# Kernel tuning notes

Hardware: AMD Instinct MI355X
Metric: run time of the kernel (lower is better)

Reference implementation:

```python
import jax, jax.numpy as jnp
import numpy as np

N_NODES = 100000
N_EDGES = 3200000
IN_FEAT = 512
HIDDEN = 16
N_CLASSES = 7


def gcn_conv(x, src, dst, dinv, W, b, n):
    # x: [N, Fin], src/dst: [E+N] (self-loops appended), dinv: [E+N already-indexed? no]
    h = x @ W  # [N, Fout]
    norm = (dinv[src] * dinv[dst])[:, None]  # [E+N, 1]
    msg = h[src] * norm
    out = jax.ops.segment_sum(msg, dst, num_segments=n)
    return out + b


def setup_inputs() -> dict:
    key = jax.random.key(0)
    k1, k2, k3, k4 = jax.random.split(key, 4)
    x = jax.random.normal(k1, (N_NODES, IN_FEAT), dtype=jnp.float32)
    edge_index = jax.random.randint(k2, (2, N_EDGES), 0, N_NODES, dtype=jnp.int64)
    # Glorot-style init for GCNConv linear layers
    W1 = jax.random.normal(k3, (IN_FEAT, HIDDEN), dtype=jnp.float32) / np.sqrt(IN_FEAT)
    b1 = jnp.zeros((HIDDEN,), dtype=jnp.float32)
    W2 = jax.random.normal(k4, (HIDDEN, N_CLASSES), dtype=jnp.float32) / np.sqrt(HIDDEN)
    b2 = jnp.zeros((N_CLASSES,), dtype=jnp.float32)
    return {"x": x, "edge_index": edge_index, "W1": W1, "b1": b1, "W2": W2, "b2": b2}


def reference(x, edge_index, W1, b1, W2, b2):
    n = x.shape[0]
    loop = jnp.arange(n, dtype=edge_index.dtype)
    src = jnp.concatenate([edge_index[0], loop])  # add self-loops (PyG default)
    dst = jnp.concatenate([edge_index[1], loop])
    # symmetric normalization: deg computed on destination with self-loops
    deg = jax.ops.segment_sum(jnp.ones_like(dst, dtype=x.dtype), dst, num_segments=n)
    dinv = jnp.where(deg > 0, jax.lax.rsqrt(deg), 0.0)
    h = gcn_conv(x, src, dst, dinv, W1, b1, n)
    h = jax.nn.relu(h)
    h = gcn_conv(h, src, dst, dinv, W2, b2, n)
    return jax.nn.log_softmax(h, axis=1)
```

## Files before the change

kernel.cpp:

```cpp
#include <hip/hip_runtime.h>

#define IN_FEAT 512
#define HID 16
#define NC 7

#define NPB    128
#define NPB_SH 7
#define NBMAX  1024
#define CAPB   5120
#define CAPS   8192
#define P1_EDGES 8192
#define P1_EPT   32

typedef float fv4 __attribute__((ext_vector_type(4)));

__global__ __launch_bounds__(256) void k_bin2(const int* __restrict__ src,
                                              const int* __restrict__ dst,
                                              int* __restrict__ gcur,
                                              int* __restrict__ binned,
                                              int E, int NB) {
    __shared__ int lcur[NBMAX];
    __shared__ int sbase[NBMAX];
    int tid = threadIdx.x;
    for (int b = tid; b < NB; b += 256) lcur[b] = 0;
    __syncthreads();

    int base = blockIdx.x * P1_EDGES + tid;
    int d[P1_EPT];
    int lp[P1_EPT];
#pragma unroll
    for (int i = 0; i < P1_EPT; ++i) {
        int e = base + i * 256;
        d[i] = (e < E) ? __builtin_nontemporal_load(dst + e) : -1;
    }
#pragma unroll
    for (int i = 0; i < P1_EPT; ++i) {
        if (d[i] >= 0) lp[i] = atomicAdd(&lcur[d[i] >> NPB_SH], 1);
    }
    __syncthreads();
    for (int b = tid; b < NB; b += 256) {
        int c = lcur[b];
        sbase[b] = c ? atomicAdd(&gcur[b], c) : 0;
    }
    __syncthreads();
#pragma unroll
    for (int i = 0; i < P1_EPT; ++i) {
        if (d[i] < 0) continue;
        int e = base + i * 256;
        int s = __builtin_nontemporal_load(src + e);
        int b = d[i] >> NPB_SH;
        int pos = sbase[b] + lp[i];
        if (pos < CAPB)
            binned[(size_t)b * CAPB + pos] = s | ((d[i] & (NPB - 1)) << 20);
    }
}

__global__ __launch_bounds__(1024) void k_bscan(const int* __restrict__ gcur,
                                                int* __restrict__ boff,
                                                int* __restrict__ off,
                                                int NB, int n, int E) {
    __shared__ int wsum[16];
    int tid = threadIdx.x, lane = tid & 63, wid = tid >> 6;
    int v = (tid < NB) ? gcur[tid] : 0;
    int incl = v;
#pragma unroll
    for (int o = 1; o < 64; o <<= 1) {
        int t = __shfl_up(incl, o, 64);
        if (lane >= o) incl += t;
    }
    if (lane == 63) wsum[wid] = incl;
    __syncthreads();
    int wpre = 0;
    for (int k = 0; k < wid; ++k) wpre += wsum[k];
    int ex = wpre + incl - v;
    if (tid < NB) boff[tid] = ex;
    if (tid == 0) off[n] = E;
}

__global__ __launch_bounds__(256) void k_sort2(const int* __restrict__ binned,
                                               const int* __restrict__ gcur,
                                               const int* __restrict__ boff,
                                               int* __restrict__ off,
                                               float* __restrict__ dinv,
                                               int* __restrict__ csr,
                                               const int* __restrict__ src,
                                               const int* __restrict__ dst,
                                               int n, int E) {
    __shared__ int hist[NPB];
    __shared__ int hoff[NPB];
    __shared__ int cur[NPB];
    __shared__ int wtot[2];
    __shared__ int stage[CAPS];
    int b = blockIdx.x;
    int lo = b << NPB_SH;
    int nn = min(NPB, n - lo);
    int tid = threadIdx.x;
    int tot = gcur[b];
    int base = boff[b];
    bool fits = (tot <= CAPB) && (tot <= CAPS);
    if (tid < NPB) { hist[tid] = 0; cur[tid] = 0; }
    __syncthreads();

    const int* bb = binned + (size_t)b * CAPB;
    if (fits) {
        for (int k = tid; k < tot; k += 256)
            atomicAdd(&hist[(bb[k] >> 20) & (NPB - 1)], 1);
    } else {
        for (int e = tid; e < E; e += 256) {
            int dd = dst[e];
            if ((dd >> NPB_SH) == b) atomicAdd(&hist[dd & (NPB - 1)], 1);
        }
    }
    __syncthreads();

    int v = 0, incl = 0;
    if (tid < NPB) {
        v = hist[tid];
        incl = v;
#pragma unroll
        for (int o = 1; o < 64; o <<= 1) {
            int t = __shfl_up(incl, o, 64);
            if ((tid & 63) >= o) incl += t;
        }
        if ((tid & 63) == 63) wtot[tid >> 6] = incl;
    }
    __syncthreads();
    if (tid < NPB) {
        int ex = incl - v + ((tid >= 64) ? wtot[0] : 0);
        hoff[tid] = ex;
        if (tid < nn) {
            off[lo + tid] = base + ex;
            dinv[lo + tid] = rsqrtf((float)v + 1.0f);
        }
    }
    __syncthreads();

    if (fits) {
        for (int k = tid; k < tot; k += 256) {
            int e = bb[k];
            int dl = (e >> 20) & (NPB - 1);
            int p = hoff[dl] + atomicAdd(&cur[dl], 1);
            stage[p] = e & 0xFFFFF;
        }
        __syncthreads();
        for (int k = tid; k < tot; k += 256) csr[base + k] = stage[k];
    } else {
        for (int e = tid; e < E; e += 256) {
            int dd = dst[e];
            if ((dd >> NPB_SH) == b) {
                int dl = dd & (NPB - 1);
                int p = base + hoff[dl] + atomicAdd(&cur[dl], 1);
                csr[p] = src[e];
            }
        }
    }
}

__global__ void k_gemm1(const float* __restrict__ x, const float* __restrict__ W,
                        float* __restrict__ h1, int n) {
    int row = blockIdx.x * blockDim.x + threadIdx.x;
    if (row >= n) return;
    const float4* xr = reinterpret_cast<const float4*>(x + (size_t)row * IN_FEAT);
    float acc[HID];
#pragma unroll
    for (int c = 0; c < HID; ++c) acc[c] = 0.0f;
    for (int kt0 = 0; kt0 < IN_FEAT / 4; kt0 += 8) {
        float4 xv[8];
#pragma unroll
        for (int j = 0; j < 8; ++j) xv[j] = xr[kt0 + j];
#pragma unroll
        for (int j = 0; j < 8; ++j) {
            const float* wk = W + (size_t)(kt0 + j) * 4 * HID;
#pragma unroll
            for (int c = 0; c < HID; ++c) acc[c] = fmaf(xv[j].x, wk[c], acc[c]);
#pragma unroll
            for (int c = 0; c < HID; ++c) acc[c] = fmaf(xv[j].y, wk[HID + c], acc[c]);
#pragma unroll
            for (int c = 0; c < HID; ++c) acc[c] = fmaf(xv[j].z, wk[2 * HID + c], acc[c]);
#pragma unroll
            for (int c = 0; c < HID; ++c) acc[c] = fmaf(xv[j].w, wk[3 * HID + c], acc[c]);
        }
    }
    float4* hp = reinterpret_cast<float4*>(h1 + (size_t)row * HID);
#pragma unroll
    for (int j = 0; j < 4; ++j)
        hp[j] = make_float4(acc[4 * j], acc[4 * j + 1], acc[4 * j + 2], acc[4 * j + 3]);
}

__global__ void k_gather1(const float* __restrict__ h1, const int* __restrict__ csr_src,
                          const int* __restrict__ off, const float* __restrict__ dinv,
                          const float* __restrict__ b1, const float* __restrict__ W2,
                          float* __restrict__ h2, int n) {
    int t = blockIdx.x * blockDim.x + threadIdx.x;
    int v = t >> 2, part = t & 3;
    if (v >= n) return;
    float di = dinv[v];
    float4 hv = reinterpret_cast<const float4*>(h1 + (size_t)v * HID)[part];
    float dw = di * di;
    float4 acc = make_float4(hv.x * dw, hv.y * dw, hv.z * dw, hv.w * dw);
    int beg = off[v], end = off[v + 1];
    for (int i = beg; i < end; ++i) {
        int s = csr_src[i];
        float w = dinv[s] * di;
        float4 hs = reinterpret_cast<const float4*>(h1 + (size_t)s * HID)[part];
        acc.x = fmaf(hs.x, w, acc.x);
        acc.y = fmaf(hs.y, w, acc.y);
        acc.z = fmaf(hs.z, w, acc.z);
        acc.w = fmaf(hs.w, w, acc.w);
    }
    float tt[4];
    tt[0] = fmaxf(acc.x + b1[part * 4 + 0], 0.0f);
    tt[1] = fmaxf(acc.y + b1[part * 4 + 1], 0.0f);
    tt[2] = fmaxf(acc.z + b1[part * 4 + 2], 0.0f);
    tt[3] = fmaxf(acc.w + b1[part * 4 + 3], 0.0f);
    float o[NC];
#pragma unroll
    for (int c = 0; c < NC; ++c) o[c] = 0.0f;
#pragma unroll
    for (int j = 0; j < 4; ++j) {
        int k = part * 4 + j;
#pragma unroll
        for (int c = 0; c < NC; ++c) o[c] = fmaf(tt[j], W2[k * NC + c], o[c]);
    }
#pragma unroll
    for (int c = 0; c < NC; ++c) {
        o[c] += __shfl_xor(o[c], 1);
        o[c] += __shfl_xor(o[c], 2);
    }
    float4* hp = reinterpret_cast<float4*>(h2 + (size_t)v * 8);
    if (part == 0) hp[0] = make_float4(o[0], o[1], o[2], o[3]);
    if (part == 1) hp[1] = make_float4(o[4], o[5], o[6], 0.0f);
}

__global__ void k_gather2(const float* __restrict__ h2, const int* __restrict__ csr_src,
                          const int* __restrict__ off, const float* __restrict__ dinv,
                          const float* __restrict__ b2, float* __restrict__ out, int n) {
    int v = blockIdx.x * blockDim.x + threadIdx.x;
    if (v >= n) return;
    float di = dinv[v];
    float dw = di * di;
    const float4* hr = reinterpret_cast<const float4*>(h2 + (size_t)v * 8);
    float4 s0 = hr[0], s1 = hr[1];
    float4 a0 = make_float4(s0.x * dw, s0.y * dw, s0.z * dw, s0.w * dw);
    float4 a1 = make_float4(s1.x * dw, s1.y * dw, s1.z * dw, 0.0f);
    int beg = off[v], end = off[v + 1];
    for (int i = beg; i < end; ++i) {
        int s = csr_src[i];
        float w = dinv[s] * di;
        const float4* hs = reinterpret_cast<const float4*>(h2 + (size_t)s * 8);
        float4 v0 = hs[0], v1 = hs[1];
        a0.x = fmaf(v0.x, w, a0.x);
        a0.y = fmaf(v0.y, w, a0.y);
        a0.z = fmaf(v0.z, w, a0.z);
        a0.w = fmaf(v0.w, w, a0.w);
        a1.x = fmaf(v1.x, w, a1.x);
        a1.y = fmaf(v1.y, w, a1.y);
        a1.z = fmaf(v1.z, w, a1.z);
    }
    float z[NC];
    z[0] = a0.x + b2[0]; z[1] = a0.y + b2[1]; z[2] = a0.z + b2[2]; z[3] = a0.w + b2[3];
    z[4] = a1.x + b2[4]; z[5] = a1.y + b2[5]; z[6] = a1.z + b2[6];
    float m = z[0];
#pragma unroll
    for (int c = 1; c < NC; ++c) m = fmaxf(m, z[c]);
    float sum = 0.0f;
#pragma unroll
    for (int c = 0; c < NC; ++c) sum += expf(z[c] - m);
    float lse = logf(sum) + m;
#pragma unroll
    for (int c = 0; c < NC; ++c) out[(size_t)v * NC + c] = z[c] - lse;
}

extern "C" void kernel_launch(void* const* d_in, const int* in_sizes, int n_in,
                              void* d_out, int out_size, void* d_ws, size_t ws_size,
                              hipStream_t stream) {
    const float* x  = (const float*)d_in[0];
    const int*   ei = (const int*)d_in[1];
    const float* W1 = (const float*)d_in[2];
    const float* b1 = (const float*)d_in[3];
    const float* W2 = (const float*)d_in[4];
    const float* b2 = (const float*)d_in[5];

    int n = in_sizes[0] / IN_FEAT;
    int E = in_sizes[1] / 2;
    const int* src = ei;
    const int* dst = ei + E;
    int NB = (n + NPB - 1) >> NPB_SH;

    char* p = (char*)d_ws;
    int*   binned  = (int*)p;
    float* h1      = (float*)p;   p += (size_t)NB * CAPB * sizeof(int);
    float* h2      = h1 + (size_t)HID * n;
    int*   csr_src = (int*)p;     p += (size_t)E * sizeof(int);
    int*   gcur    = (int*)p;     p += (size_t)NBMAX * sizeof(int);
    int*   boff    = (int*)p;     p += (size_t)NBMAX * sizeof(int);
    int*   off     = (int*)p;     p += (size_t)(n + 1) * sizeof(int);
    float* dinv    = (float*)p;   p += (size_t)n * sizeof(float);

    const int tb = 256;
    int gN = (n + tb - 1) / tb;
    int gN4 = (4 * n + tb - 1) / tb;
    int nchunk = (E + P1_EDGES - 1) / P1_EDGES;

    hipMemsetAsync(gcur, 0, (size_t)NBMAX * sizeof(int), stream);
    k_bin2   <<<nchunk, tb, 0, stream>>>(src, dst, gcur, binned, E, NB);
    k_bscan  <<<1, 1024, 0, stream>>>(gcur, boff, off, NB, n, E);
    k_sort2  <<<NB, tb, 0, stream>>>(binned, gcur, boff, off, dinv, csr_src,
                                     src, dst, n, E);
    k_gemm1  <<<gN,  tb, 0, stream>>>(x, W1, h1, n);
    k_gather1<<<gN4, tb, 0, stream>>>(h1, csr_src, off, dinv, b1, W2, h2, n);
    k_gather2<<<gN,  tb, 0, stream>>>(h2, csr_src, off, dinv, b2, (float*)d_out, n);
}
```

Measured before the change: 266.9 us.

## Merge edge binning with first GEMM and fold bin scan into sort

The edge-binning kernel and the x@W1 GEMM now run as one horizontally fused launch, with block index choosing the role, so the two independent phases can overlap on the GPU. The separate single-block prefix-scan kernel is removed: each sort block sums the preceding bin counts itself with a strided loop and wavefront reduction. h1 no longer aliases the binned buffer, which makes the overlap safe at the cost of extra workspace. The change removes two launches and their gaps but adds redundant prefix work in every sort block.

```diff
diff --git a/kernel.cpp b/kernel.cpp
--- a/kernel.cpp
+++ b/kernel.cpp
@@ -12,94 +12,112 @@
 #define P1_EDGES 8192
 #define P1_EPT   32
 
-typedef float fv4 __attribute__((ext_vector_type(4)));
-
-__global__ __launch_bounds__(256) void k_bin2(const int* __restrict__ src,
-                                              const int* __restrict__ dst,
-                                              int* __restrict__ gcur,
-                                              int* __restrict__ binned,
-                                              int E, int NB) {
-    __shared__ int lcur[NBMAX];
-    __shared__ int sbase[NBMAX];
+__global__ __launch_bounds__(256) void k_binmm(const int* __restrict__ src,
+                                               const int* __restrict__ dst,
+                                               int* __restrict__ gcur,
+                                               int* __restrict__ binned,
+                                               const float* __restrict__ x,
+                                               const float* __restrict__ W,
+                                               float* __restrict__ h1,
+                                               int E, int NB, int nchunk, int n) {
     int tid = threadIdx.x;
-    for (int b = tid; b < NB; b += 256) lcur[b] = 0;
-    __syncthreads();
-
-    int base = blockIdx.x * P1_EDGES + tid;
-    int d[P1_EPT];
-    int lp[P1_EPT];
-#pragma unroll
-    for (int i = 0; i < P1_EPT; ++i) {
-        int e = base + i * 256;
-        d[i] = (e < E) ? __builtin_nontemporal_load(dst + e) : -1;
-    }
-#pragma unroll
-    for (int i = 0; i < P1_EPT; ++i) {
-        if (d[i] >= 0) lp[i] = atomicAdd(&lcur[d[i] >> NPB_SH], 1);
-    }
-    __syncthreads();
-    for (int b = tid; b < NB; b += 256) {
-        int c = lcur[b];
-        sbase[b] = c ? atomicAdd(&gcur[b], c) : 0;
-    }
-    __syncthreads();
-#pragma unroll
-    for (int i = 0; i < P1_EPT; ++i) {
-        if (d[i] < 0) continue;
-        int e = base + i * 256;
-        int s = __builtin_nontemporal_load(src + e);
-        int b = d[i] >> NPB_SH;
-        int pos = sbase[b] + lp[i];
-        if (pos < CAPB)
-            binned[(size_t)b * CAPB + pos] = s | ((d[i] & (NPB - 1)) << 20);
-    }
-}
-
-__global__ __launch_bounds__(1024) void k_bscan(const int* __restrict__ gcur,
-                                                int* __restrict__ boff,
-                                                int* __restrict__ off,
-                                                int NB, int n, int E) {
-    __shared__ int wsum[16];
-    int tid = threadIdx.x, lane = tid & 63, wid = tid >> 6;
-    int v = (tid < NB) ? gcur[tid] : 0;
-    int incl = v;
-#pragma unroll
-    for (int o = 1; o < 64; o <<= 1) {
-        int t = __shfl_up(incl, o, 64);
-        if (lane >= o) incl += t;
-    }
-    if (lane == 63) wsum[wid] = incl;
-    __syncthreads();
-    int wpre = 0;
-    for (int k = 0; k < wid; ++k) wpre += wsum[k];
-    int ex = wpre + incl - v;
-    if (tid < NB) boff[tid] = ex;
-    if (tid == 0) off[n] = E;
+    if ((int)blockIdx.x < nchunk) {
+        __shared__ int lcur[NBMAX];
+        __shared__ int sbase[NBMAX];
+        for (int b = tid; b < NB; b += 256) lcur[b] = 0;
+        __syncthreads();
+
+        int base = blockIdx.x * P1_EDGES + tid;
+        int d[P1_EPT];
+        int lp[P1_EPT];
+#pragma unroll
+        for (int i = 0; i < P1_EPT; ++i) {
+            int e = base + i * 256;
+            d[i] = (e < E) ? __builtin_nontemporal_load(dst + e) : -1;
+        }
+#pragma unroll
+        for (int i = 0; i < P1_EPT; ++i) {
+            if (d[i] >= 0) lp[i] = atomicAdd(&lcur[d[i] >> NPB_SH], 1);
+        }
+        __syncthreads();
+        for (int b = tid; b < NB; b += 256) {
+            int c = lcur[b];
+            sbase[b] = c ? atomicAdd(&gcur[b], c) : 0;
+        }
+        __syncthreads();
+#pragma unroll
+        for (int i = 0; i < P1_EPT; ++i) {
+            if (d[i] < 0) continue;
+            int e = base + i * 256;
+            int s = __builtin_nontemporal_load(src + e);
+            int b = d[i] >> NPB_SH;
+            int pos = sbase[b] + lp[i];
+            if (pos < CAPB)
+                binned[(size_t)b * CAPB + pos] = s | ((d[i] & (NPB - 1)) << 20);
+        }
+    } else {
+        int row = ((int)blockIdx.x - nchunk) * 256 + tid;
+        if (row >= n) return;
+        const float4* xr = reinterpret_cast<const float4*>(x + (size_t)row * IN_FEAT);
+        float acc[HID];
+#pragma unroll
+        for (int c = 0; c < HID; ++c) acc[c] = 0.0f;
+        for (int kt0 = 0; kt0 < IN_FEAT / 4; kt0 += 8) {
+            float4 xv[8];
+#pragma unroll
+            for (int j = 0; j < 8; ++j) xv[j] = xr[kt0 + j];
+#pragma unroll
+            for (int j = 0; j < 8; ++j) {
+                const float* wk = W + (size_t)(kt0 + j) * 4 * HID;
+#pragma unroll
+                for (int c = 0; c < HID; ++c) acc[c] = fmaf(xv[j].x, wk[c], acc[c]);
+#pragma unroll
+                for (int c = 0; c < HID; ++c) acc[c] = fmaf(xv[j].y, wk[HID + c], acc[c]);
+#pragma unroll
+                for (int c = 0; c < HID; ++c) acc[c] = fmaf(xv[j].z, wk[2 * HID + c], acc[c]);
+#pragma unroll
+                for (int c = 0; c < HID; ++c) acc[c] = fmaf(xv[j].w, wk[3 * HID + c], acc[c]);
+            }
+        }
+        float4* hp = reinterpret_cast<float4*>(h1 + (size_t)row * HID);
+#pragma unroll
+        for (int j = 0; j < 4; ++j)
+            hp[j] = make_float4(acc[4 * j], acc[4 * j + 1], acc[4 * j + 2], acc[4 * j + 3]);
+    }
 }
 
 __global__ __launch_bounds__(256) void k_sort2(const int* __restrict__ binned,
                                                const int* __restrict__ gcur,
-                                               const int* __restrict__ boff,
                                                int* __restrict__ off,
                                                float* __restrict__ dinv,
                                                int* __restrict__ csr,
                                                const int* __restrict__ src,
                                                const int* __restrict__ dst,
-                                               int n, int E) {
+                                               int n, int E, int NB) {
     __shared__ int hist[NPB];
     __shared__ int hoff[NPB];
     __shared__ int cur[NPB];
-    __shared__ int wtot[2];
+    __shared__ int wtot[4];
+    __shared__ int s_base;
     __shared__ int stage[CAPS];
     int b = blockIdx.x;
     int lo = b << NPB_SH;
     int nn = min(NPB, n - lo);
     int tid = threadIdx.x;
+    int lane = tid & 63, wid = tid >> 6;
     int tot = gcur[b];
-    int base = boff[b];
+
+    int pre = 0;
+    for (int k = tid; k < b; k += 256) pre += gcur[k];
+#pragma unroll
+    for (int o = 32; o >= 1; o >>= 1) pre += __shfl_xor(pre, o, 64);
+    if (lane == 0) wtot[wid] = pre;
+    if (tid < NPB) { hist[tid] = 0; cur[tid] = 0; }
+    __syncthreads();
+    if (tid == 0) s_base = wtot[0] + wtot[1] + wtot[2] + wtot[3];
+    __syncthreads();
+    int base = s_base;
     bool fits = (tot <= CAPB) && (tot <= CAPS);
-    if (tid < NPB) { hist[tid] = 0; cur[tid] = 0; }
-    __syncthreads();
 
     const int* bb = binned + (size_t)b * CAPB;
     if (fits) {
@@ -133,6 +151,7 @@
             dinv[lo + tid] = rsqrtf((float)v + 1.0f);
         }
     }
+    if (b == NB - 1 && tid == 0) off[n] = base + tot;
     __syncthreads();
 
     if (fits) {
@@ -154,37 +173,6 @@
             }
         }
     }
-}
-
-__global__ void k_gemm1(const float* __restrict__ x, const float* __restrict__ W,
-                        float* __restrict__ h1, int n) {
-    int row = blockIdx.x * blockDim.x + threadIdx.x;
-    if (row >= n) return;
-    const float4* xr = reinterpret_cast<const float4*>(x + (size_t)row * IN_FEAT);
-    float acc[HID];
-#pragma unroll
-    for (int c = 0; c < HID; ++c) acc[c] = 0.0f;
-    for (int kt0 = 0; kt0 < IN_FEAT / 4; kt0 += 8) {
-        float4 xv[8];
-#pragma unroll
-        for (int j = 0; j < 8; ++j) xv[j] = xr[kt0 + j];
-#pragma unroll
-        for (int j = 0; j < 8; ++j) {
-            const float* wk = W + (size_t)(kt0 + j) * 4 * HID;
-#pragma unroll
-            for (int c = 0; c < HID; ++c) acc[c] = fmaf(xv[j].x, wk[c], acc[c]);
-#pragma unroll
-            for (int c = 0; c < HID; ++c) acc[c] = fmaf(xv[j].y, wk[HID + c], acc[c]);
-#pragma unroll
-            for (int c = 0; c < HID; ++c) acc[c] = fmaf(xv[j].z, wk[2 * HID + c], acc[c]);
-#pragma unroll
-            for (int c = 0; c < HID; ++c) acc[c] = fmaf(xv[j].w, wk[3 * HID + c], acc[c]);
-        }
-    }
-    float4* hp = reinterpret_cast<float4*>(h1 + (size_t)row * HID);
-#pragma unroll
-    for (int j = 0; j < 4; ++j)
-        hp[j] = make_float4(acc[4 * j], acc[4 * j + 1], acc[4 * j + 2], acc[4 * j + 3]);
 }
 
 __global__ void k_gather1(const float* __restrict__ h1, const int* __restrict__ csr_src,
@@ -288,12 +276,11 @@
     int NB = (n + NPB - 1) >> NPB_SH;
 
     char* p = (char*)d_ws;
-    int*   binned  = (int*)p;
-    float* h1      = (float*)p;   p += (size_t)NB * CAPB * sizeof(int);
-    float* h2      = h1 + (size_t)HID * n;
+    int*   binned  = (int*)p;     p += (size_t)NB * CAPB * sizeof(int);
+    float* h1      = (float*)p;   p += (size_t)HID * n * sizeof(float);
+    float* h2      = (float*)p;   p += (size_t)8 * n * sizeof(float);
     int*   csr_src = (int*)p;     p += (size_t)E * sizeof(int);
     int*   gcur    = (int*)p;     p += (size_t)NBMAX * sizeof(int);
-    int*   boff    = (int*)p;     p += (size_t)NBMAX * sizeof(int);
     int*   off     = (int*)p;     p += (size_t)(n + 1) * sizeof(int);
     float* dinv    = (float*)p;   p += (size_t)n * sizeof(float);
 
@@ -303,11 +290,10 @@
     int nchunk = (E + P1_EDGES - 1) / P1_EDGES;
 
     hipMemsetAsync(gcur, 0, (size_t)NBMAX * sizeof(int), stream);
-    k_bin2   <<<nchunk, tb, 0, stream>>>(src, dst, gcur, binned, E, NB);
-    k_bscan  <<<1, 1024, 0, stream>>>(gcur, boff, off, NB, n, E);
-    k_sort2  <<<NB, tb, 0, stream>>>(binned, gcur, boff, off, dinv, csr_src,
-                                     src, dst, n, E);
-    k_gemm1  <<<gN,  tb, 0, stream>>>(x, W1, h1, n);
+    k_binmm  <<<nchunk + gN, tb, 0, stream>>>(src, dst, gcur, binned, x, W1, h1,
+                                              E, NB, nchunk, n);
+    k_sort2  <<<NB, tb, 0, stream>>>(binned, gcur, off, dinv, csr_src,
+                                     src, dst, n, E, NB);
     k_gather1<<<gN4, tb, 0, stream>>>(h1, csr_src, off, dinv, b1, W2, h2, n);
     k_gather2<<<gN,  tb, 0, stream>>>(h2, csr_src, off, dinv, b2, (float*)d_out, n);
 }
```

New measurement: 253.5 us. 1.05x faster.
